# Kernel optimization log

Hardware: AMD Instinct MI355X
Metric: run time of the kernel (lower is better)

The kernel has to match this reference:

```python
import jax, jax.numpy as jnp
import numpy as np
import math

D_MODEL = 1024
NHEAD = 16
FACTOR = 5


def setup_inputs() -> dict:
    key = jax.random.key(0)
    ks = jax.random.split(key, 9)
    d = D_MODEL
    s = 1.0 / math.sqrt(d)
    x = jax.random.normal(ks[0], (2, 2048, d), dtype=jnp.float32)
    Wq = jax.random.normal(ks[1], (d, d), dtype=jnp.float32) * s
    bq = jnp.zeros((d,), dtype=jnp.float32)
    Wk = jax.random.normal(ks[2], (d, d), dtype=jnp.float32) * s
    bk = jnp.zeros((d,), dtype=jnp.float32)
    Wv = jax.random.normal(ks[3], (d, d), dtype=jnp.float32) * s
    bv = jnp.zeros((d,), dtype=jnp.float32)
    Wo = jax.random.normal(ks[4], (d, d), dtype=jnp.float32) * s
    bo = jnp.zeros((d,), dtype=jnp.float32)
    return {"x": x, "Wq": Wq, "bq": bq, "Wk": Wk, "bk": bk,
            "Wv": Wv, "bv": bv, "Wo": Wo, "bo": bo}


def reference(x, Wq, bq, Wk, bk, Wv, bv, Wo, bo):
    B, L, d_model = x.shape
    H = NHEAD
    D = d_model // H
    # U = min(L, int(factor * log(L)))  (static, L > 1)
    U = min(L, int(FACTOR * math.log(L)))

    def proj(W, b):
        # [B,L,d] -> [B,H,L,D]
        return (x @ W.T + b).reshape(B, L, H, D).transpose(0, 2, 1, 3)

    Q = proj(Wq, bq)
    K = proj(Wk, bk)
    V = proj(Wv, bv)

    scores = jnp.einsum('bhqd,bhkd->bhqk', Q, K) / math.sqrt(D)  # [B,H,L,L]
    top_vals, _ = jax.lax.top_k(scores, U)                       # [B,H,L,U]
    thresh = top_vals[..., -1:]                                  # kth largest per row
    scores = jnp.where(scores < thresh, -jnp.inf, scores)
    attn = jax.nn.softmax(scores, axis=-1)                       # dropout p=0 (eval)
    context = jnp.einsum('bhqk,bhkd->bhqd', attn, V)             # [B,H,L,D]
    context = context.transpose(0, 2, 1, 3).reshape(B, L, d_model)
    return context @ Wo.T + bo
```

## Files before the change

kernel.cpp:

```cpp
#include <hip/hip_runtime.h>
#include <math.h>

#define B_SZ 2
#define L_SEQ 2048
#define NH 16
#define HD 64
#define DM 1024
#define TQ 8
#define DELTA 1.2e-5f
#define CAP 224
#define NCAND 16

__global__ __launch_bounds__(256)
void gemm_nt(const float* __restrict__ A, const float* __restrict__ W,
             const float* __restrict__ bias, float* __restrict__ C,
             int M, int N, int K, int mode)
{
    __shared__ float As[2][16][132];
    __shared__ float Bs[2][16][132];
    int tid = threadIdx.x;
    int bn = blockIdx.x * 128;
    int bm = blockIdx.y * 128;
    int tm = tid >> 4, tn = tid & 15;
    int lr = tid >> 1, lk = (tid & 1) * 8;

    const float* Ag = A + (size_t)(bm + lr) * K + lk;
    const float* Bg = W + (size_t)(bn + lr) * K + lk;

    float acc[8][8] = {};

    float4 a0 = *(const float4*)(Ag + 0);
    float4 a1 = *(const float4*)(Ag + 4);
    float4 b0 = *(const float4*)(Bg + 0);
    float4 b1 = *(const float4*)(Bg + 4);
    As[0][lk+0][lr]=a0.x; As[0][lk+1][lr]=a0.y; As[0][lk+2][lr]=a0.z; As[0][lk+3][lr]=a0.w;
    As[0][lk+4][lr]=a1.x; As[0][lk+5][lr]=a1.y; As[0][lk+6][lr]=a1.z; As[0][lk+7][lr]=a1.w;
    Bs[0][lk+0][lr]=b0.x; Bs[0][lk+1][lr]=b0.y; Bs[0][lk+2][lr]=b0.z; Bs[0][lk+3][lr]=b0.w;
    Bs[0][lk+4][lr]=b1.x; Bs[0][lk+5][lr]=b1.y; Bs[0][lk+6][lr]=b1.z; Bs[0][lk+7][lr]=b1.w;
    __syncthreads();

    int cur = 0;
    for (int k0 = 0; k0 < K; k0 += 16) {
        bool nxt = (k0 + 16) < K;
        if (nxt) {
            a0 = *(const float4*)(Ag + k0 + 16);
            a1 = *(const float4*)(Ag + k0 + 20);
            b0 = *(const float4*)(Bg + k0 + 16);
            b1 = *(const float4*)(Bg + k0 + 20);
        }
        #pragma unroll
        for (int kk = 0; kk < 16; ++kk) {
            float4 aA = *(const float4*)&As[cur][kk][tm*8];
            float4 aB = *(const float4*)&As[cur][kk][tm*8+4];
            float4 bA = *(const float4*)&Bs[cur][kk][tn*8];
            float4 bB = *(const float4*)&Bs[cur][kk][tn*8+4];
            float av[8] = {aA.x,aA.y,aA.z,aA.w,aB.x,aB.y,aB.z,aB.w};
            float bv[8] = {bA.x,bA.y,bA.z,bA.w,bB.x,bB.y,bB.z,bB.w};
            #pragma unroll
            for (int i = 0; i < 8; ++i)
                #pragma unroll
                for (int j = 0; j < 8; ++j)
                    acc[i][j] += av[i] * bv[j];
        }
        if (nxt) {
            int nb = cur ^ 1;
            As[nb][lk+0][lr]=a0.x; As[nb][lk+1][lr]=a0.y; As[nb][lk+2][lr]=a0.z; As[nb][lk+3][lr]=a0.w;
            As[nb][lk+4][lr]=a1.x; As[nb][lk+5][lr]=a1.y; As[nb][lk+6][lr]=a1.z; As[nb][lk+7][lr]=a1.w;
            Bs[nb][lk+0][lr]=b0.x; Bs[nb][lk+1][lr]=b0.y; Bs[nb][lk+2][lr]=b0.z; Bs[nb][lk+3][lr]=b0.w;
            Bs[nb][lk+4][lr]=b1.x; Bs[nb][lk+5][lr]=b1.y; Bs[nb][lk+6][lr]=b1.z; Bs[nb][lk+7][lr]=b1.w;
            __syncthreads();
            cur = nb;
        }
    }

    #pragma unroll
    for (int i = 0; i < 8; ++i) {
        int r = bm + tm*8 + i;
        #pragma unroll
        for (int j4 = 0; j4 < 8; j4 += 4) {
            int c = bn + tn*8 + j4;
            float4 v;
            v.x = acc[i][j4+0]; v.y = acc[i][j4+1];
            v.z = acc[i][j4+2]; v.w = acc[i][j4+3];
            if (mode == 2) {
                float bb = bias[r];
                v.x += bb; v.y += bb; v.z += bb; v.w += bb;
                int h = r >> 6,  d = r & (HD - 1);
                int b = c >> 11, l = c & (L_SEQ - 1);
                *(float4*)&C[(((size_t)(b * NH + h)) * HD + d) * L_SEQ + l] = v;
            } else {
                float4 bb = *(const float4*)&bias[c];
                v.x += bb.x; v.y += bb.y; v.z += bb.z; v.w += bb.w;
                if (mode == 0) {
                    int b = r >> 11, l = r & (L_SEQ - 1);
                    int h = c >> 6,  d = c & (HD - 1);
                    *(float4*)&C[(((size_t)(b * NH + h)) * L_SEQ + l) * HD + d] = v;
                } else {
                    *(float4*)&C[(size_t)r * N + c] = v;
                }
            }
        }
    }
}

__global__ __launch_bounds__(512, 4)
void attn_topk(const float* __restrict__ Q, const float* __restrict__ KT,
               const float* __restrict__ V, float* __restrict__ ctx, int U)
{
    __shared__ float sc[TQ][L_SEQ];
    __shared__ float qs[TQ][HD];
    __shared__ float lp[TQ][CAP];
    __shared__ short lidx[TQ][CAP];
    __shared__ int   hist[TQ][66];

    int tid = threadIdx.x;
    int nb  = gridDim.x;
    int lb  = (blockIdx.x & 7) * (nb >> 3) + (blockIdx.x >> 3);
    int bh  = lb >> 8;
    int qt  = lb & 255;
    int q0  = qt * TQ;

    const float* KTb = KT + (size_t)bh * HD * L_SEQ;
    const float* Vb  = V  + (size_t)bh * L_SEQ * HD;

    {
        int r = tid >> 6, d = tid & 63;
        qs[r][d] = Q[((size_t)bh * L_SEQ + q0 + r) * HD + d] * 0.125f;
    }
    __syncthreads();

    {
        int k4 = tid * 4;
        float4 acc[TQ];
        #pragma unroll
        for (int r = 0; r < TQ; ++r) acc[r] = make_float4(0.f, 0.f, 0.f, 0.f);
        #pragma unroll 4
        for (int d0 = 0; d0 < HD; d0 += 4) {
            float4 qv[TQ];
            #pragma unroll
            for (int r = 0; r < TQ; ++r) qv[r] = *(const float4*)&qs[r][d0];
            #pragma unroll
            for (int dd = 0; dd < 4; ++dd) {
                float4 kt = *(const float4*)(KTb + (size_t)(d0 + dd) * L_SEQ + k4);
                #pragma unroll
                for (int r = 0; r < TQ; ++r) {
                    float q = (dd == 0) ? qv[r].x : (dd == 1) ? qv[r].y
                            : (dd == 2) ? qv[r].z : qv[r].w;
                    acc[r].x += q * kt.x; acc[r].y += q * kt.y;
                    acc[r].z += q * kt.z; acc[r].w += q * kt.w;
                }
            }
        }
        #pragma unroll
        for (int r = 0; r < TQ; ++r)
            *(float4*)&sc[r][k4] = acc[r];
    }
    __syncthreads();

    int wv   = tid >> 6;
    int lane = tid & 63;

    float f[32];
    #pragma unroll
    for (int i = 0; i < 32; ++i)
        f[i] = sc[wv][lane + 64 * i];

    float lmax = -3.402823466e38f;
    #pragma unroll
    for (int i = 0; i < 32; ++i) lmax = fmaxf(lmax, f[i]);
    float mx = lmax, Aanch = lmax;
    #pragma unroll
    for (int m = 32; m; m >>= 1) {
        mx    = fmaxf(mx,    __shfl_xor(mx,    m));
        Aanch = fminf(Aanch, __shfl_xor(Aanch, m));
    }

    float Ln = Aanch;
    float w  = fmaxf(mx - Aanch, 1e-30f);

    {
        float hinv = 62.0f / w;
        hist[wv][lane] = 0;
        if (lane < 2) hist[wv][64 + lane] = 0;
        #pragma unroll
        for (int i = 0; i < 32; ++i) {
            float g = fminf((f[i] - Ln) * hinv + 1.0f, 64.5f);
            if (g >= 0.5f) atomicAdd(&hist[wv][(int)g], 1);
        }
        int v = hist[wv][lane] + ((lane == 63) ? hist[wv][64] : 0);
        #pragma unroll
        for (int d = 1; d < 64; d <<= 1) {
            int t = __shfl_down(v, d);
            if (lane + d < 64) v += t;
        }
        unsigned long long m2 = __ballot(v >= U);
        int bstar = 63 - __clzll((long long)m2);
        if (bstar < 0) bstar = 0;
        float w62 = w * (1.0f / 62.0f);
        Ln = Ln + (float)(bstar - 1) * w62;
        w  = w62;
    }

    float cf[NCAND];
    int nc = 0;
    #pragma unroll
    for (int i = 0; i < 32; ++i) {
        if (f[i] >= Ln) {
            if (nc < NCAND) cf[nc] = f[i];
            nc++;
        }
    }
    bool ovf = __ballot(nc > NCAND) != 0ull;

    for (int pass = 0; pass < 3; ++pass) {
        float hinv = 62.0f / w;
        hist[wv][lane] = 0;
        if (lane < 2) hist[wv][64 + lane] = 0;
        if (!ovf) {
            int n = nc < NCAND ? nc : NCAND;
            for (int j = 0; j < n; ++j) {
                float g = fminf((cf[j] - Ln) * hinv + 1.0f, 64.5f);
                if (g >= 0.5f) atomicAdd(&hist[wv][(int)g], 1);
            }
        } else {
            #pragma unroll
            for (int i = 0; i < 32; ++i) {
                float g = fminf((f[i] - Ln) * hinv + 1.0f, 64.5f);
                if (g >= 0.5f) atomicAdd(&hist[wv][(int)g], 1);
            }
        }
        int v = hist[wv][lane] + ((lane == 63) ? hist[wv][64] : 0);
        #pragma unroll
        for (int d = 1; d < 64; d <<= 1) {
            int t = __shfl_down(v, d);
            if (lane + d < 64) v += t;
        }
        unsigned long long m2 = __ballot(v >= U);
        int bstar = 63 - __clzll((long long)m2);
        if (bstar < 0) bstar = 0;
        float w62 = w * (1.0f / 62.0f);
        Ln = Ln + (float)(bstar - 1) * w62;
        w  = w62;
    }
    float tlo = Ln - w - DELTA;
    float thi = Ln + 2.0f * w + DELTA;

    int rcnt = 0, ccnt = 0, nl = 0;
    unsigned selbits = 0;
    #pragma unroll
    for (int i = 0; i < 32; ++i) {
        bool hi = f[i] > thi;
        bool in = f[i] >= tlo;
        rcnt += hi ? 1 : 0;
        ccnt += (in && !hi) ? 1 : 0;
        if (in) { selbits |= 1u << i; nl++; }
    }
    int pack = (rcnt << 16) | ccnt;
    #pragma unroll
    for (int m = 32; m; m >>= 1) pack += __shfl_xor(pack, m);
    rcnt = pack >> 16; ccnt = pack & 0xFFFF;
    float wm = (float)(U - rcnt) / (float)ccnt;

    int incl = nl;
    #pragma unroll
    for (int d = 1; d < 64; d <<= 1) {
        int v = __shfl_up(incl, d);
        if (lane >= d) incl += v;
    }
    int total = __shfl(incl, 63);
    int off = incl - nl;

    float psum = 0.f;
    unsigned sb = selbits;
    while (sb) {
        int i = __builtin_ctz(sb);
        sb &= sb - 1;
        float wk = (f[i] > thi) ? 1.f : wm;
        float p  = wk * __expf(f[i] - mx);
        psum += p;
        if (off < CAP) {
            lp[wv][off]   = p;
            lidx[wv][off] = (short)(lane + 64 * i);
        }
        off++;
    }
    #pragma unroll
    for (int m = 32; m; m >>= 1) psum += __shfl_xor(psum, m);
    float inv = 1.f / psum;

    int n = total < CAP ? total : CAP;
    float acc = 0.f;
    for (int i = 0; i < n; ++i) {
        float p = lp[wv][i];
        int   k = lidx[wv][i];
        acc += p * Vb[(size_t)k * HD + lane];
    }
    int b = bh >> 4, h = bh & (NH - 1);
    int q = q0 + wv;
    ctx[(((size_t)(b * L_SEQ + q)) * NH + h) * HD + lane] = acc * inv;
}

extern "C" void kernel_launch(void* const* d_in, const int* in_sizes, int n_in,
                              void* d_out, int out_size, void* d_ws, size_t ws_size,
                              hipStream_t stream)
{
    const float* x  = (const float*)d_in[0];
    const float* Wq = (const float*)d_in[1];
    const float* bq = (const float*)d_in[2];
    const float* Wk = (const float*)d_in[3];
    const float* bk = (const float*)d_in[4];
    const float* Wv = (const float*)d_in[5];
    const float* bv = (const float*)d_in[6];
    const float* Wo = (const float*)d_in[7];
    const float* bo = (const float*)d_in[8];
    float* out = (float*)d_out;

    const int M = B_SZ * L_SEQ;
    const int N = DM;
    const int K = DM;

    size_t per = (size_t)M * DM;
    float* Qw  = (float*)d_ws;
    float* KTw = Qw + per;
    float* Vw  = KTw + per;
    float* Cw  = Vw + per;

    int U = (int)(5.0 * log((double)L_SEQ));
    if (U > L_SEQ) U = L_SEQ;

    dim3 blk(256);

    hipLaunchKernelGGL(gemm_nt, dim3(N / 128, M / 128), blk, 0, stream,
                       x, Wq, bq, Qw, M, N, K, 0);
    hipLaunchKernelGGL(gemm_nt, dim3(M / 128, N / 128), blk, 0, stream,
                       Wk, x, bk, KTw, N, M, K, 2);
    hipLaunchKernelGGL(gemm_nt, dim3(N / 128, M / 128), blk, 0, stream,
                       x, Wv, bv, Vw, M, N, K, 0);

    hipLaunchKernelGGL(attn_topk, dim3(B_SZ * NH * (L_SEQ / TQ)), dim3(512),
                       0, stream, Qw, KTw, Vw, Cw, U);

    hipLaunchKernelGGL(gemm_nt, dim3(N / 128, M / 128), blk, 0, stream,
                       Cw, Wo, bo, out, M, N, K, 1);
}
```

Baseline: 989.9 us.

## Merge QKV GEMMs into one launch and halve GEMM tile width to 128x64

```diff
diff --git a/kernel.cpp b/kernel.cpp
--- a/kernel.cpp
+++ b/kernel.cpp
@@ -11,32 +11,28 @@
 #define CAP 224
 #define NCAND 16
 
-__global__ __launch_bounds__(256)
-void gemm_nt(const float* __restrict__ A, const float* __restrict__ W,
-             const float* __restrict__ bias, float* __restrict__ C,
-             int M, int N, int K, int mode)
-{
-    __shared__ float As[2][16][132];
-    __shared__ float Bs[2][16][132];
-    int tid = threadIdx.x;
-    int bn = blockIdx.x * 128;
-    int bm = blockIdx.y * 128;
+__device__ __forceinline__ void gemm_core(
+    const float* __restrict__ A, const float* __restrict__ W,
+    const float* __restrict__ bias, float* __restrict__ C,
+    int bm, int bn, int mode, int tid,
+    float As[2][16][132], float Bs[2][16][68])
+{
+    const int K = DM;
     int tm = tid >> 4, tn = tid & 15;
-    int lr = tid >> 1, lk = (tid & 1) * 8;
-
-    const float* Ag = A + (size_t)(bm + lr) * K + lk;
-    const float* Bg = W + (size_t)(bn + lr) * K + lk;
-
-    float acc[8][8] = {};
+    int lrA = tid >> 1, lkA = (tid & 1) * 8;
+    int lrB = tid >> 2, lkB = (tid & 3) * 4;
+
+    const float* Ag = A + (size_t)(bm + lrA) * K + lkA;
+    const float* Bg = W + (size_t)(bn + lrB) * K + lkB;
+
+    float acc[8][4] = {};
 
     float4 a0 = *(const float4*)(Ag + 0);
     float4 a1 = *(const float4*)(Ag + 4);
     float4 b0 = *(const float4*)(Bg + 0);
-    float4 b1 = *(const float4*)(Bg + 4);
-    As[0][lk+0][lr]=a0.x; As[0][lk+1][lr]=a0.y; As[0][lk+2][lr]=a0.z; As[0][lk+3][lr]=a0.w;
-    As[0][lk+4][lr]=a1.x; As[0][lk+5][lr]=a1.y; As[0][lk+6][lr]=a1.z; As[0][lk+7][lr]=a1.w;
-    Bs[0][lk+0][lr]=b0.x; Bs[0][lk+1][lr]=b0.y; Bs[0][lk+2][lr]=b0.z; Bs[0][lk+3][lr]=b0.w;
-    Bs[0][lk+4][lr]=b1.x; Bs[0][lk+5][lr]=b1.y; Bs[0][lk+6][lr]=b1.z; Bs[0][lk+7][lr]=b1.w;
+    As[0][lkA+0][lrA]=a0.x; As[0][lkA+1][lrA]=a0.y; As[0][lkA+2][lrA]=a0.z; As[0][lkA+3][lrA]=a0.w;
+    As[0][lkA+4][lrA]=a1.x; As[0][lkA+5][lrA]=a1.y; As[0][lkA+6][lrA]=a1.z; As[0][lkA+7][lrA]=a1.w;
+    Bs[0][lkB+0][lrB]=b0.x; Bs[0][lkB+1][lrB]=b0.y; Bs[0][lkB+2][lrB]=b0.z; Bs[0][lkB+3][lrB]=b0.w;
     __syncthreads();
 
     int cur = 0;
@@ -46,61 +42,94 @@
             a0 = *(const float4*)(Ag + k0 + 16);
             a1 = *(const float4*)(Ag + k0 + 20);
             b0 = *(const float4*)(Bg + k0 + 16);
-            b1 = *(const float4*)(Bg + k0 + 20);
         }
         #pragma unroll
         for (int kk = 0; kk < 16; ++kk) {
             float4 aA = *(const float4*)&As[cur][kk][tm*8];
             float4 aB = *(const float4*)&As[cur][kk][tm*8+4];
-            float4 bA = *(const float4*)&Bs[cur][kk][tn*8];
-            float4 bB = *(const float4*)&Bs[cur][kk][tn*8+4];
+            float4 bA = *(const float4*)&Bs[cur][kk][tn*4];
             float av[8] = {aA.x,aA.y,aA.z,aA.w,aB.x,aB.y,aB.z,aB.w};
-            float bv[8] = {bA.x,bA.y,bA.z,bA.w,bB.x,bB.y,bB.z,bB.w};
+            float bv[4] = {bA.x,bA.y,bA.z,bA.w};
             #pragma unroll
             for (int i = 0; i < 8; ++i)
                 #pragma unroll
-                for (int j = 0; j < 8; ++j)
+                for (int j = 0; j < 4; ++j)
                     acc[i][j] += av[i] * bv[j];
         }
         if (nxt) {
-            int nb = cur ^ 1;
-            As[nb][lk+0][lr]=a0.x; As[nb][lk+1][lr]=a0.y; As[nb][lk+2][lr]=a0.z; As[nb][lk+3][lr]=a0.w;
-            As[nb][lk+4][lr]=a1.x; As[nb][lk+5][lr]=a1.y; As[nb][lk+6][lr]=a1.z; As[nb][lk+7][lr]=a1.w;
-            Bs[nb][lk+0][lr]=b0.x; Bs[nb][lk+1][lr]=b0.y; Bs[nb][lk+2][lr]=b0.z; Bs[nb][lk+3][lr]=b0.w;
-            Bs[nb][lk+4][lr]=b1.x; Bs[nb][lk+5][lr]=b1.y; Bs[nb][lk+6][lr]=b1.z; Bs[nb][lk+7][lr]=b1.w;
+            int nb2 = cur ^ 1;
+            As[nb2][lkA+0][lrA]=a0.x; As[nb2][lkA+1][lrA]=a0.y; As[nb2][lkA+2][lrA]=a0.z; As[nb2][lkA+3][lrA]=a0.w;
+            As[nb2][lkA+4][lrA]=a1.x; As[nb2][lkA+5][lrA]=a1.y; As[nb2][lkA+6][lrA]=a1.z; As[nb2][lkA+7][lrA]=a1.w;
+            Bs[nb2][lkB+0][lrB]=b0.x; Bs[nb2][lkB+1][lrB]=b0.y; Bs[nb2][lkB+2][lrB]=b0.z; Bs[nb2][lkB+3][lrB]=b0.w;
             __syncthreads();
-            cur = nb;
+            cur = nb2;
         }
     }
 
     #pragma unroll
     for (int i = 0; i < 8; ++i) {
         int r = bm + tm*8 + i;
-        #pragma unroll
-        for (int j4 = 0; j4 < 8; j4 += 4) {
-            int c = bn + tn*8 + j4;
-            float4 v;
-            v.x = acc[i][j4+0]; v.y = acc[i][j4+1];
-            v.z = acc[i][j4+2]; v.w = acc[i][j4+3];
-            if (mode == 2) {
-                float bb = bias[r];
-                v.x += bb; v.y += bb; v.z += bb; v.w += bb;
-                int h = r >> 6,  d = r & (HD - 1);
-                int b = c >> 11, l = c & (L_SEQ - 1);
-                *(float4*)&C[(((size_t)(b * NH + h)) * HD + d) * L_SEQ + l] = v;
+        int c = bn + tn*4;
+        float4 v;
+        v.x = acc[i][0]; v.y = acc[i][1]; v.z = acc[i][2]; v.w = acc[i][3];
+        if (mode == 2) {
+            float bb = bias[r];
+            v.x += bb; v.y += bb; v.z += bb; v.w += bb;
+            int h = r >> 6,  d = r & (HD - 1);
+            int b = c >> 11, l = c & (L_SEQ - 1);
+            *(float4*)&C[(((size_t)(b * NH + h)) * HD + d) * L_SEQ + l] = v;
+        } else {
+            float4 bb = *(const float4*)&bias[c];
+            v.x += bb.x; v.y += bb.y; v.z += bb.z; v.w += bb.w;
+            if (mode == 0) {
+                int b = r >> 11, l = r & (L_SEQ - 1);
+                int h = c >> 6,  d = c & (HD - 1);
+                *(float4*)&C[(((size_t)(b * NH + h)) * L_SEQ + l) * HD + d] = v;
             } else {
-                float4 bb = *(const float4*)&bias[c];
-                v.x += bb.x; v.y += bb.y; v.z += bb.z; v.w += bb.w;
-                if (mode == 0) {
-                    int b = r >> 11, l = r & (L_SEQ - 1);
-                    int h = c >> 6,  d = c & (HD - 1);
-                    *(float4*)&C[(((size_t)(b * NH + h)) * L_SEQ + l) * HD + d] = v;
-                } else {
-                    *(float4*)&C[(size_t)r * N + c] = v;
-                }
+                *(float4*)&C[(size_t)r * DM + c] = v;
             }
         }
     }
+}
+
+__global__ __launch_bounds__(256)
+void qkv_gemm(const float* __restrict__ x,
+              const float* __restrict__ Wq, const float* __restrict__ bq,
+              const float* __restrict__ Wk, const float* __restrict__ bk,
+              const float* __restrict__ Wv, const float* __restrict__ bv,
+              float* __restrict__ Qw, float* __restrict__ KTw, float* __restrict__ Vw)
+{
+    __shared__ float As[2][16][132];
+    __shared__ float Bs[2][16][68];
+    int bid = blockIdx.x;
+    int z  = bid >> 9;
+    int rb = bid & 511;
+    int tid = threadIdx.x;
+
+    const float *A, *W, *bias;
+    float* C;
+    int bm, bn, mode;
+    if (z == 1) {
+        A = Wk; W = x; bias = bk; C = KTw; mode = 2;
+        bm = (rb >> 6) * 128;
+        bn = (rb & 63) * 64;
+    } else {
+        A = x; bias = (z == 0) ? bq : bv; W = (z == 0) ? Wq : Wv;
+        C = (z == 0) ? Qw : Vw; mode = 0;
+        bm = (rb >> 4) * 128;
+        bn = (rb & 15) * 64;
+    }
+    gemm_core(A, W, bias, C, bm, bn, mode, tid, As, Bs);
+}
+
+__global__ __launch_bounds__(256)
+void out_gemm(const float* __restrict__ Cw, const float* __restrict__ Wo,
+              const float* __restrict__ bo, float* __restrict__ out)
+{
+    __shared__ float As[2][16][132];
+    __shared__ float Bs[2][16][68];
+    gemm_core(Cw, Wo, bo, out, blockIdx.y * 128, blockIdx.x * 64, 1,
+              threadIdx.x, As, Bs);
 }
 
 __global__ __launch_bounds__(512, 4)
@@ -315,11 +344,7 @@
     const float* bo = (const float*)d_in[8];
     float* out = (float*)d_out;
 
-    const int M = B_SZ * L_SEQ;
-    const int N = DM;
-    const int K = DM;
-
-    size_t per = (size_t)M * DM;
+    size_t per = (size_t)(B_SZ * L_SEQ) * DM;
     float* Qw  = (float*)d_ws;
     float* KTw = Qw + per;
     float* Vw  = KTw + per;
@@ -328,18 +353,12 @@
     int U = (int)(5.0 * log((double)L_SEQ));
     if (U > L_SEQ) U = L_SEQ;
 
-    dim3 blk(256);
-
-    hipLaunchKernelGGL(gemm_nt, dim3(N / 128, M / 128), blk, 0, stream,
-                       x, Wq, bq, Qw, M, N, K, 0);
-    hipLaunchKernelGGL(gemm_nt, dim3(M / 128, N / 128), blk, 0, stream,
-                       Wk, x, bk, KTw, N, M, K, 2);
-    hipLaunchKernelGGL(gemm_nt, dim3(N / 128, M / 128), blk, 0, stream,
-                       x, Wv, bv, Vw, M, N, K, 0);
+    hipLaunchKernelGGL(qkv_gemm, dim3(3 * 512), dim3(256), 0, stream,
+                       x, Wq, bq, Wk, bk, Wv, bv, Qw, KTw, Vw);
 
     hipLaunchKernelGGL(attn_topk, dim3(B_SZ * NH * (L_SEQ / TQ)), dim3(512),
                        0, stream, Qw, KTw, Vw, Cw, U);
 
-    hipLaunchKernelGGL(gemm_nt, dim3(N / 128, M / 128), blk, 0, stream,
-                       Cw, Wo, bo, out, M, N, K, 1);
-}
+    hipLaunchKernelGGL(out_gemm, dim3(16, 32), dim3(256), 0, stream,
+                       Cw, Wo, bo, out);
+}
```

After: 976.2 us. Within noise of the previous version (-1.4%).
